# Performance work log

Hardware: AMD Instinct MI355X
Metric: run time of the kernel (lower is better)

The kernel has to match this reference:

```python
import jax, jax.numpy as jnp
import numpy as np

HIDDEN = 1024
CUTOFFS = [20000, 80000, 200000]
PROJECT_FACTOR = 4
NUM_TAILS = len(CUTOFFS) - 1
CUTOFF_ENDS = [0] + CUTOFFS
BATCH, SEQ = 8, 1024


def _glorot(key, shape):
    fan_in, fan_out = shape
    limit = np.sqrt(6.0 / (fan_in + fan_out)).astype(np.float32)
    return jax.random.uniform(key, shape, jnp.float32, -limit, limit)


def setup_inputs() -> dict:
    key = jax.random.key(0)
    ks = jax.random.split(key, 7)
    return {
        "x": jax.random.randint(ks[0], (BATCH, SEQ), 0, CUTOFFS[-1], dtype=jnp.int64.dtype if jax.config.jax_enable_x64 else jnp.int32),
        "head_weight_proj": _glorot(ks[1], (HIDDEN, HIDDEN)),
        "head_weight": _glorot(ks[2], (HIDDEN, CUTOFFS[0] + NUM_TAILS)),
        "tail_weight_proj_0": _glorot(ks[3], (HIDDEN, HIDDEN // PROJECT_FACTOR)),
        "tail_weight_0": _glorot(ks[4], (HIDDEN // PROJECT_FACTOR, CUTOFFS[1] - CUTOFFS[0])),
        "tail_weight_proj_1": _glorot(ks[5], (HIDDEN, HIDDEN // PROJECT_FACTOR ** 2)),
        "tail_weight_1": _glorot(ks[6], (HIDDEN // PROJECT_FACTOR ** 2, CUTOFFS[2] - CUTOFFS[1])),
    }


def reference(x, head_weight_proj, head_weight, tail_weight_proj_0,
              tail_weight_0, tail_weight_proj_1, tail_weight_1) -> jnp.ndarray:
    # Faithful to AdaptiveEmbedding.compute_embeddings:
    #   tables[i] = weight.T (head truncated to cutoffs[0] rows), projs[i] = proj.T
    #   per-cluster: gather rows of table for in-range ids, matmul with proj,
    #   scatter back into y; here expressed densely with masks (same math,
    #   fixed shapes; out-of-cluster tokens contribute exactly zero).
    tables = [head_weight.T[:CUTOFFS[0]], tail_weight_0.T, tail_weight_1.T]
    projs = [head_weight_proj.T, tail_weight_proj_0.T, tail_weight_proj_1.T]
    y = jnp.zeros(x.shape + (HIDDEN,), dtype=jnp.float32)
    for i in range(len(CUTOFF_ENDS) - 1):
        l_idx, r_idx = CUTOFF_ENDS[i], CUTOFF_ENDS[i + 1]
        mask = (x >= l_idx) & (x < r_idx)                  # [B,S]
        idx = jnp.where(mask, x - l_idx, 0)                # in-range gather ids
        emb = tables[i][idx]                               # [B,S,d_i]
        proj = jnp.einsum('bsd,dh->bsh', emb, projs[i])    # [B,S,H]
        y = y + jnp.where(mask[..., None], proj, 0.0)
    emb_scale = jnp.asarray(HIDDEN ** 0.5, y.dtype)
    return y * emb_scale
```

## Files before the change

kernel.cpp:

```cpp
#include <hip/hip_runtime.h>
#include <hip/hip_bf16.h>

#define NTOK 8192
#define HID 1024
#define C0_END 20000
#define C1_END 80000
#define S0 20002
#define S1 60000
#define S2 120000

#define CAP0 1280
#define CAP1 3072
#define CAP2 6144
#define TS0 (CAP0/32)
#define TS1 (CAP1/32)
#define TS2 (CAP2/32)

#define NBUCK 12500

#define OFF_CNT 0
#define OFF_SST 16
#define OFF_BB  32
#define OFF_LS  50048
#define OFF_LI  (OFF_LS + NTOK*3*4)
#define OFF_W0  (OFF_LI + NTOK*3*4)
#define OFF_W1  (OFF_W0 + 1024*1024*2)
#define OFF_W2  (OFF_W1 + 256*1024*2)
#define OFF_A0  (OFF_W2 + 64*1024*2)
#define OFF_A1  (OFF_A0 + CAP0*1024*2)
#define OFF_A2  (OFF_A1 + CAP1*256*2)

typedef __attribute__((ext_vector_type(8))) short bf16x8;
typedef __attribute__((ext_vector_type(4))) float f32x4;

__device__ __forceinline__ unsigned short f2bf(float f) {
    union { __hip_bfloat16 b; unsigned short u; } cv;
    cv.b = __float2bfloat16(f);
    return cv.u;
}


__global__ void k_init(unsigned* __restrict__ bb, int* __restrict__ cnt) {
    int gid = blockIdx.x * 256 + threadIdx.x, stride = gridDim.x * 256;
    for (int i = gid; i < NBUCK; i += stride) bb[i] = 0u;
    if (gid < 3) cnt[gid] = 0;
}

__global__ void k_count(const int* __restrict__ x, int* __restrict__ cnt,
                        unsigned* __restrict__ bb) {
    int s = blockIdx.x * 256 + threadIdx.x;
    int lane = threadIdx.x & 63;
    int v = x[s];
    atomicAdd(&bb[v >> 4], 1u);
    int c = (v < C0_END) ? 0 : (v < C1_END ? 1 : 2);
    unsigned long long m0 = __ballot(c == 0);
    unsigned long long m1 = __ballot(c == 1);
    unsigned long long m2 = __ballot(c == 2);
    unsigned long long mymask = (c == 0) ? m0 : (c == 1) ? m1 : m2;
    int leader = __builtin_ctzll(mymask);
    if (lane == leader) atomicAdd(&cnt[c], __popcll(mymask));
}

__global__ __launch_bounds__(1024) void k_scan(unsigned* __restrict__ bb,
                                               unsigned* __restrict__ sstart) {
    __shared__ unsigned psum[16];
    int t = threadIdx.x, lane = t & 63, w = t >> 6;
    int base = t * 13;
    unsigned loc[13];
    unsigned s = 0;
#pragma unroll
    for (int i = 0; i < 13; i++) {
        int idx = base + i;
        unsigned v = (idx < NBUCK) ? bb[idx] : 0u;
        loc[i] = v; s += v;
    }
    unsigned inc = s;
    for (int d = 1; d < 64; d <<= 1) {
        unsigned o = __shfl_up(inc, d);
        if (lane >= d) inc += o;
    }
    if (lane == 63) psum[w] = inc;
    __syncthreads();
    if (w == 0) {
        unsigned ws = (lane < 16) ? psum[lane] : 0u;
        for (int d = 1; d < 16; d <<= 1) {
            unsigned o = __shfl_up(ws, d);
            if (lane >= d) ws += o;
        }
        if (lane < 16) psum[lane] = ws;
    }
    __syncthreads();
    unsigned excl = inc - s + ((w > 0) ? psum[w - 1] : 0u);
#pragma unroll
    for (int i = 0; i < 13; i++) {
        int idx = base + i;
        if (idx < NBUCK) bb[idx] = excl;
        excl += loc[i];
    }
    __syncthreads();
    if (t == 0) { sstart[0] = 0u; sstart[1] = bb[1250]; sstart[2] = bb[5000]; }
}

__global__ void k_scatter(const int* __restrict__ x, unsigned* __restrict__ bb,
                          const unsigned* __restrict__ sstart,
                          int* __restrict__ ls, int* __restrict__ li) {
    int s = blockIdx.x * 256 + threadIdx.x;
    int v = x[s];
    int c    = (v < C0_END) ? 0 : (v < C1_END ? 1 : 2);
    int base = (c == 0) ? 0 : (c == 1) ? C0_END : C1_END;
    unsigned cap = (c == 0) ? CAP0 : (c == 1) ? CAP1 : CAP2;
    unsigned pos = atomicAdd(&bb[v >> 4], 1u) - sstart[c];
    if (pos < cap) {
        ls[c * NTOK + pos] = s;
        li[c * NTOK + pos] = v - base;
    }
}

template <int KS>
__device__ __forceinline__ size_t frag_off(int m, int k8) {
    return ((size_t)(((m >> 5) * KS + (k8 >> 2)) * 2 + ((m >> 4) & 1)) << 9)
         + (size_t)(((m & 15) + (k8 & 3) * 16) * 8);
}

template <int KS, int K16, int SHIFT, int S>
__device__ __forceinline__ void gather_item(int itL, int lane, int n,
                                            const float* __restrict__ t,
                                            const int* __restrict__ li,
                                            unsigned short* __restrict__ A) {
    int k16 = itL & (K16 - 1);
    int tw  = itL >> SHIFT;
    int m   = tw * 4 + (lane & 3);
    int row = k16 * 16 + (lane >> 2);
    int idx = (m < n) ? li[m] : 0;
    float x = t[(size_t)row * S + idx];
    unsigned v = (m < n) ? (unsigned)f2bf(x) : 0u;
    int h = (lane >> 2) & 1, tt = lane & 3;
    unsigned p[8];
#pragma unroll
    for (int jj = 0; jj < 8; jj++) {
        int sl = (((h * 8 + jj) * 4) + tt) * 4;
        p[jj] = (unsigned)__builtin_amdgcn_ds_bpermute(sl, (int)v);
    }
    if (lane < 8) {
        unsigned q0 = (p[0] & 0xFFFFu) | (p[1] << 16);
        unsigned q1 = (p[2] & 0xFFFFu) | (p[3] << 16);
        unsigned q2 = (p[4] & 0xFFFFu) | (p[5] << 16);
        unsigned q3 = (p[6] & 0xFFFFu) | (p[7] << 16);
        int mo = tw * 4 + tt;
        int k8 = k16 * 2 + h;
        uint4 q = { q0, q1, q2, q3 };
        *(uint4*)(A + frag_off<KS>(mo, k8)) = q;
    }
}

__global__ void k_gather(const float* __restrict__ t0, const float* __restrict__ t1,
                         const float* __restrict__ t2,
                         const float* __restrict__ hwp, const float* __restrict__ twp0,
                         const float* __restrict__ twp1,
                         const int* __restrict__ cnt, const int* __restrict__ li,
                         unsigned short* __restrict__ A0, unsigned short* __restrict__ A1,
                         unsigned short* __restrict__ A2,
                         unsigned short* __restrict__ W0, unsigned short* __restrict__ W1,
                         unsigned short* __restrict__ W2) {
    int gid = blockIdx.x * 256 + threadIdx.x, stride = gridDim.x * 256;
    for (int i = gid; i < (1024 * 1024) / 4; i += stride) {
        float4 v = ((const float4*)hwp)[i];
        ushort4 o = { f2bf(v.x), f2bf(v.y), f2bf(v.z), f2bf(v.w) };
        ((ushort4*)W0)[i] = o;
    }
    for (int i = gid; i < (1024 * 256) / 4; i += stride) {
        float4 v = ((const float4*)twp0)[i];
        ushort4 o = { f2bf(v.x), f2bf(v.y), f2bf(v.z), f2bf(v.w) };
        ((ushort4*)W1)[i] = o;
    }
    for (int i = gid; i < (1024 * 64) / 4; i += stride) {
        float4 v = ((const float4*)twp1)[i];
        ushort4 o = { f2bf(v.x), f2bf(v.y), f2bf(v.z), f2bf(v.w) };
        ((ushort4*)W2)[i] = o;
    }
    int n0 = min(cnt[0], CAP0), n1 = min(cnt[1], CAP1), n2 = min(cnt[2], CAP2);
    int r0 = ((n0 + 31) >> 5) << 5;
    int r1 = ((n1 + 31) >> 5) << 5;
    int r2 = ((n2 + 31) >> 5) << 5;
    int i0 = (r0 >> 2) << 6;
    int i1 = (r1 >> 2) << 4;
    int i2 = (r2 >> 2) << 2;
    int tot = i0 + i1 + i2;
    int lane = threadIdx.x & 63;
    int wid = blockIdx.x * (blockDim.x >> 6) + (threadIdx.x >> 6);
    int nw  = gridDim.x * (blockDim.x >> 6);
    for (int it = wid; it < tot; it += nw) {
        if (it < i0)
            gather_item<32, 64, 6, S0>(it, lane, n0, t0, li, A0);
        else if (it < i0 + i1)
            gather_item<8, 16, 4, S1>(it - i0, lane, n1, t1, li + NTOK, A1);
        else
            gather_item<2, 4, 2, S2>(it - i0 - i1, lane, n2, t2, li + 2 * NTOK, A2);
    }
}

template <int K>
__device__ __forceinline__ void gemm_body(int tile, int n, int lane, int wave, int by,
                                          const unsigned short* __restrict__ Ap,
                                          const unsigned short* __restrict__ Wb,
                                          const int* __restrict__ ls,
                                          float* __restrict__ out) {
    constexpr int KS = K / 32;
    int m0 = tile * 32;
    int lr = lane & 15, lg = lane >> 4;
    int hb = by * 256 + wave * 64;
    const unsigned short* abase = Ap + (size_t)tile * KS * 1024 + lane * 8;
    const unsigned short* bbase = Wb + (size_t)(hb + lr) * K + lg * 8;
    f32x4 acc[2][4] = {};
#pragma unroll 4
    for (int ks = 0; ks < KS; ks++) {
        bf16x8 a0 = *(const bf16x8*)(abase + ks * 1024);
        bf16x8 a1 = *(const bf16x8*)(abase + ks * 1024 + 512);
        bf16x8 b0 = *(const bf16x8*)(bbase + ks * 32);
        bf16x8 b1 = *(const bf16x8*)(bbase + ks * 32 + 16 * K);
        bf16x8 b2 = *(const bf16x8*)(bbase + ks * 32 + 32 * K);
        bf16x8 b3 = *(const bf16x8*)(bbase + ks * 32 + 48 * K);
        acc[0][0] = __builtin_amdgcn_mfma_f32_16x16x32_bf16(a0, b0, acc[0][0], 0, 0, 0);
        acc[0][1] = __builtin_amdgcn_mfma_f32_16x16x32_bf16(a0, b1, acc[0][1], 0, 0, 0);
        acc[0][2] = __builtin_amdgcn_mfma_f32_16x16x32_bf16(a0, b2, acc[0][2], 0, 0, 0);
        acc[0][3] = __builtin_amdgcn_mfma_f32_16x16x32_bf16(a0, b3, acc[0][3], 0, 0, 0);
        acc[1][0] = __builtin_amdgcn_mfma_f32_16x16x32_bf16(a1, b0, acc[1][0], 0, 0, 0);
        acc[1][1] = __builtin_amdgcn_mfma_f32_16x16x32_bf16(a1, b1, acc[1][1], 0, 0, 0);
        acc[1][2] = __builtin_amdgcn_mfma_f32_16x16x32_bf16(a1, b2, acc[1][2], 0, 0, 0);
        acc[1][3] = __builtin_amdgcn_mfma_f32_16x16x32_bf16(a1, b3, acc[1][3], 0, 0, 0);
    }
#pragma unroll
    for (int mf = 0; mf < 2; mf++)
#pragma unroll
        for (int r = 0; r < 4; r++) {
            int m = mf * 16 + lg * 4 + r;
            if (m0 + m < n) {
                int s = ls[m0 + m];
                float* orow = out + (size_t)s * HID + hb + lr;
                orow[0]  = 32.f * acc[mf][0][r];
                orow[16] = 32.f * acc[mf][1][r];
                orow[32] = 32.f * acc[mf][2][r];
                orow[48] = 32.f * acc[mf][3][r];
            }
        }
}

__global__ __launch_bounds__(256) void k_gemm(const int* __restrict__ cnt,
                                              const int* __restrict__ ls,
                                              const unsigned short* __restrict__ A0,
                                              const unsigned short* __restrict__ A1,
                                              const unsigned short* __restrict__ A2,
                                              const unsigned short* __restrict__ W0,
                                              const unsigned short* __restrict__ W1,
                                              const unsigned short* __restrict__ W2,
                                              float* __restrict__ out) {
    int bx = blockIdx.x;
    int lane = threadIdx.x & 63, wave = threadIdx.x >> 6;
    if (bx < TS0) {
        int n = min(cnt[0], CAP0); if (bx * 32 >= n) return;
        gemm_body<1024>(bx, n, lane, wave, blockIdx.y, A0, W0, ls, out);
    } else if (bx < TS0 + TS1) {
        int t = bx - TS0;
        int n = min(cnt[1], CAP1); if (t * 32 >= n) return;
        gemm_body<256>(t, n, lane, wave, blockIdx.y, A1, W1, ls + NTOK, out);
    } else {
        int t = bx - TS0 - TS1;
        int n = min(cnt[2], CAP2); if (t * 32 >= n) return;
        gemm_body<64>(t, n, lane, wave, blockIdx.y, A2, W2, ls + 2 * NTOK, out);
    }
}

extern "C" void kernel_launch(void* const* d_in, const int* in_sizes, int n_in,
                              void* d_out, int out_size, void* d_ws, size_t ws_size,
                              hipStream_t stream) {
    const int*   x    = (const int*)d_in[0];
    const float* hwp  = (const float*)d_in[1];
    const float* hw   = (const float*)d_in[2];
    const float* twp0 = (const float*)d_in[3];
    const float* tw0  = (const float*)d_in[4];
    const float* twp1 = (const float*)d_in[5];
    const float* tw1  = (const float*)d_in[6];

    char* ws = (char*)d_ws;
    int* cnt          = (int*)(ws + OFF_CNT);
    unsigned* sstart  = (unsigned*)(ws + OFF_SST);
    unsigned* bb      = (unsigned*)(ws + OFF_BB);
    int* ls           = (int*)(ws + OFF_LS);
    int* li           = (int*)(ws + OFF_LI);
    unsigned short* W0 = (unsigned short*)(ws + OFF_W0);
    unsigned short* W1 = (unsigned short*)(ws + OFF_W1);
    unsigned short* W2 = (unsigned short*)(ws + OFF_W2);
    unsigned short* A0 = (unsigned short*)(ws + OFF_A0);
    unsigned short* A1 = (unsigned short*)(ws + OFF_A1);
    unsigned short* A2 = (unsigned short*)(ws + OFF_A2);
    float* out = (float*)d_out;

    k_init<<<64, 256, 0, stream>>>(bb, cnt);
    k_count<<<NTOK / 256, 256, 0, stream>>>(x, cnt, bb);
    k_scan<<<1, 1024, 0, stream>>>(bb, sstart);
    k_scatter<<<NTOK / 256, 256, 0, stream>>>(x, bb, sstart, ls, li);
    k_gather<<<2048, 256, 0, stream>>>(hw, tw0, tw1, hwp, twp0, twp1,
                                       cnt, li, A0, A1, A2, W0, W1, W2);
    k_gemm<<<dim3(TS0 + TS1 + TS2, 4), 256, 0, stream>>>(
        cnt, ls, A0, A1, A2, W0, W1, W2, out);
}
```

Baseline: 79.31 us.

## Replace scattered column gather with coalesced row-window extraction using bucket ranges

Measured after the change: 110.7 us. 39.6% more time.

```diff
diff --git a/kernel.cpp b/kernel.cpp
--- a/kernel.cpp
+++ b/kernel.cpp
@@ -17,6 +17,10 @@
 #define TS2 (CAP2/32)
 
 #define NBUCK 12500
+
+#define NW0 79
+#define NW1 235
+#define NW2 469
 
 #define OFF_CNT 0
 #define OFF_SST 16
@@ -116,52 +120,10 @@
     }
 }
 
-template <int KS>
-__device__ __forceinline__ size_t frag_off(int m, int k8) {
-    return ((size_t)(((m >> 5) * KS + (k8 >> 2)) * 2 + ((m >> 4) & 1)) << 9)
-         + (size_t)(((m & 15) + (k8 & 3) * 16) * 8);
-}
-
-template <int KS, int K16, int SHIFT, int S>
-__device__ __forceinline__ void gather_item(int itL, int lane, int n,
-                                            const float* __restrict__ t,
-                                            const int* __restrict__ li,
-                                            unsigned short* __restrict__ A) {
-    int k16 = itL & (K16 - 1);
-    int tw  = itL >> SHIFT;
-    int m   = tw * 4 + (lane & 3);
-    int row = k16 * 16 + (lane >> 2);
-    int idx = (m < n) ? li[m] : 0;
-    float x = t[(size_t)row * S + idx];
-    unsigned v = (m < n) ? (unsigned)f2bf(x) : 0u;
-    int h = (lane >> 2) & 1, tt = lane & 3;
-    unsigned p[8];
-#pragma unroll
-    for (int jj = 0; jj < 8; jj++) {
-        int sl = (((h * 8 + jj) * 4) + tt) * 4;
-        p[jj] = (unsigned)__builtin_amdgcn_ds_bpermute(sl, (int)v);
-    }
-    if (lane < 8) {
-        unsigned q0 = (p[0] & 0xFFFFu) | (p[1] << 16);
-        unsigned q1 = (p[2] & 0xFFFFu) | (p[3] << 16);
-        unsigned q2 = (p[4] & 0xFFFFu) | (p[5] << 16);
-        unsigned q3 = (p[6] & 0xFFFFu) | (p[7] << 16);
-        int mo = tw * 4 + tt;
-        int k8 = k16 * 2 + h;
-        uint4 q = { q0, q1, q2, q3 };
-        *(uint4*)(A + frag_off<KS>(mo, k8)) = q;
-    }
-}
-
-__global__ void k_gather(const float* __restrict__ t0, const float* __restrict__ t1,
-                         const float* __restrict__ t2,
-                         const float* __restrict__ hwp, const float* __restrict__ twp0,
-                         const float* __restrict__ twp1,
-                         const int* __restrict__ cnt, const int* __restrict__ li,
-                         unsigned short* __restrict__ A0, unsigned short* __restrict__ A1,
-                         unsigned short* __restrict__ A2,
-                         unsigned short* __restrict__ W0, unsigned short* __restrict__ W1,
-                         unsigned short* __restrict__ W2) {
+__global__ void k_convert(const float* __restrict__ hwp, const float* __restrict__ twp0,
+                          const float* __restrict__ twp1,
+                          unsigned short* __restrict__ W0, unsigned short* __restrict__ W1,
+                          unsigned short* __restrict__ W2) {
     int gid = blockIdx.x * 256 + threadIdx.x, stride = gridDim.x * 256;
     for (int i = gid; i < (1024 * 1024) / 4; i += stride) {
         float4 v = ((const float4*)hwp)[i];
@@ -178,24 +140,89 @@
         ushort4 o = { f2bf(v.x), f2bf(v.y), f2bf(v.z), f2bf(v.w) };
         ((ushort4*)W2)[i] = o;
     }
-    int n0 = min(cnt[0], CAP0), n1 = min(cnt[1], CAP1), n2 = min(cnt[2], CAP2);
-    int r0 = ((n0 + 31) >> 5) << 5;
-    int r1 = ((n1 + 31) >> 5) << 5;
-    int r2 = ((n2 + 31) >> 5) << 5;
-    int i0 = (r0 >> 2) << 6;
-    int i1 = (r1 >> 2) << 4;
-    int i2 = (r2 >> 2) << 2;
-    int tot = i0 + i1 + i2;
+}
+
+template <int KS>
+__device__ __forceinline__ size_t frag_base(int m, int k) {
+    return ((size_t)(((m >> 5) * KS + (k >> 5)) * 2 + ((m >> 4) & 1)) << 9)
+         + (size_t)((((m & 15) + (((k >> 3) & 3) << 4)) << 3) + (k & 7));
+}
+
+template <int RL2, int V, int S, int KS, int CAPC, int B0, int NBC>
+__device__ __forceinline__ void extract_item(int itL, int lane,
+                                             const float* __restrict__ t,
+                                             const unsigned* __restrict__ bbEnd,
+                                             const int* __restrict__ li,
+                                             unsigned sstc,
+                                             unsigned short* __restrict__ A) {
+    int w  = itL >> RL2;
+    int rp = itL & ((1 << RL2) - 1);
+    int r  = rp * 2;
+    int colbase = w << 8;
+    int b0 = B0 + w * 16;
+    int blast = min(b0 + 15, B0 + NBC - 1);
+    unsigned pst = (b0 == 0) ? 0u : bbEnd[b0 - 1];
+    unsigned pen = bbEnd[blast];
+    if (pen <= pst) return;
+    int colc = min(colbase + lane * 4, V - 4);
+    const float* rowp = t + (size_t)r * S + colc;
+    float4 va = *(const float4*)(rowp);
+    float4 vb = *(const float4*)(rowp + S);
+    unsigned nt = pen - pst;
+    for (unsigned ch = 0; ch < nt; ch += 64) {
+        int cnum = (int)min(64u, nt - ch);
+        int mycol = -1;
+        if (lane < cnum) {
+            int mm = (int)(pst + ch - sstc) + lane;
+            mycol = ((unsigned)mm < (unsigned)CAPC) ? li[mm] : -1;
+        }
+        for (int q = 0; q < cnum; ++q) {
+            int col = __shfl(mycol, q);
+            if (col < 0) continue;
+            int cc = col - colbase;
+            float a01 = (cc & 1) ? va.y : va.x;
+            float a23 = (cc & 1) ? va.w : va.z;
+            float as  = (cc & 2) ? a23 : a01;
+            float b01 = (cc & 1) ? vb.y : vb.x;
+            float b23 = (cc & 1) ? vb.w : vb.z;
+            float bs  = (cc & 2) ? b23 : b01;
+            float ga = __shfl(as, cc >> 2);
+            float gb = __shfl(bs, cc >> 2);
+            if (lane == q) {
+                int m = (int)(pst + ch - sstc) + q;
+                unsigned pk = (unsigned)f2bf(ga) | ((unsigned)f2bf(gb) << 16);
+                *(unsigned*)(A + frag_base<KS>(m, r)) = pk;
+            }
+        }
+    }
+}
+
+#define EX_I0 (NW0 << 9)
+#define EX_I1 (NW1 << 7)
+#define EX_I2 (NW2 << 5)
+
+__global__ void k_extract(const float* __restrict__ t0, const float* __restrict__ t1,
+                          const float* __restrict__ t2,
+                          const unsigned* __restrict__ bb,
+                          const unsigned* __restrict__ sstart,
+                          const int* __restrict__ li,
+                          unsigned short* __restrict__ A0, unsigned short* __restrict__ A1,
+                          unsigned short* __restrict__ A2) {
     int lane = threadIdx.x & 63;
+    unsigned sst1 = sstart[1], sst2 = sstart[2];
     int wid = blockIdx.x * (blockDim.x >> 6) + (threadIdx.x >> 6);
     int nw  = gridDim.x * (blockDim.x >> 6);
+    const int tot = EX_I0 + EX_I1 + EX_I2;
     for (int it = wid; it < tot; it += nw) {
-        if (it < i0)
-            gather_item<32, 64, 6, S0>(it, lane, n0, t0, li, A0);
-        else if (it < i0 + i1)
-            gather_item<8, 16, 4, S1>(it - i0, lane, n1, t1, li + NTOK, A1);
+        if (it < EX_I0)
+            extract_item<9, 20000, S0, 32, CAP0, 0, 1250>(
+                it, lane, t0, bb, li, 0u, A0);
+        else if (it < EX_I0 + EX_I1)
+            extract_item<7, 60000, S1, 8, CAP1, 1250, 3750>(
+                it - EX_I0, lane, t1, bb, li + NTOK, sst1, A1);
         else
-            gather_item<2, 4, 2, S2>(it - i0 - i1, lane, n2, t2, li + 2 * NTOK, A2);
+            extract_item<5, 120000, S2, 2, CAP2, 5000, 7500>(
+                it - EX_I0 - EX_I1, lane, t2, bb, li + 2 * NTOK, sst2, A2);
     }
 }
 
@@ -299,8 +326,8 @@
     k_count<<<NTOK / 256, 256, 0, stream>>>(x, cnt, bb);
     k_scan<<<1, 1024, 0, stream>>>(bb, sstart);
     k_scatter<<<NTOK / 256, 256, 0, stream>>>(x, bb, sstart, ls, li);
-    k_gather<<<2048, 256, 0, stream>>>(hw, tw0, tw1, hwp, twp0, twp1,
-                                       cnt, li, A0, A1, A2, W0, W1, W2);
+    k_convert<<<512, 256, 0, stream>>>(hwp, twp0, twp1, W0, W1, W2);
+    k_extract<<<2048, 256, 0, stream>>>(hw, tw0, tw1, bb, sstart, li, A0, A1, A2);
     k_gemm<<<dim3(TS0 + TS1 + TS2, 4), 256, 0, stream>>>(
         cnt, ls, A0, A1, A2, W0, W1, W2, out);
 }
```
